# Optimization experiments

Measured on AMD Instinct MI355X. Metric: run time of the kernel, lower is better.

## Reference

```python
import jax, jax.numpy as jnp
import numpy as np


def setup_inputs() -> dict:
    key = jax.random.key(0)
    ks = jax.random.split(key, 8)
    B, S, V, E, H = 64, 128, 8000, 256, 512
    scale = 0.05
    return {
        "inputs": jax.random.randint(ks[0], (B, S), 0, V, dtype=jnp.int64),
        "embedding": jax.random.normal(ks[1], (V, E), dtype=jnp.float32) * scale,
        "W_ih": jax.random.normal(ks[2], (4 * H, E), dtype=jnp.float32) * scale,
        "W_hh": jax.random.normal(ks[3], (4 * H, H), dtype=jnp.float32) * scale,
        "b_ih": jax.random.normal(ks[4], (4 * H,), dtype=jnp.float32) * scale,
        "b_hh": jax.random.normal(ks[5], (4 * H,), dtype=jnp.float32) * scale,
        "W_cls": jax.random.normal(ks[6], (V, H), dtype=jnp.float32) * scale,
        "b_cls": jax.random.normal(ks[7], (V,), dtype=jnp.float32) * scale,
    }


def reference(inputs, embedding, W_ih, W_hh, b_ih, b_hh, W_cls, b_cls):
    B, S = inputs.shape
    H = W_hh.shape[1]
    x = embedding[inputs]  # (B, S, E)
    # batch the input-to-hidden GEMM across all timesteps
    x_gates = jnp.einsum('bse,ge->bsg', x, W_ih) + b_ih + b_hh  # (B, S, 4H)

    def step(carry, xg):
        h, c = carry
        gates = xg + h @ W_hh.T  # (B, 4H)
        i, f, g, o = jnp.split(gates, 4, axis=-1)  # PyTorch LSTMCell gate order
        i = jax.nn.sigmoid(i)
        f = jax.nn.sigmoid(f)
        g = jnp.tanh(g)
        o = jax.nn.sigmoid(o)
        c = f * c + i * g
        h = o * jnp.tanh(c)
        return (h, c), h

    h0 = jnp.zeros((B, H), dtype=x.dtype)
    c0 = jnp.zeros((B, H), dtype=x.dtype)
    _, hs = jax.lax.scan(step, (h0, c0), jnp.swapaxes(x_gates, 0, 1))  # hs: (S, B, H)
    hidden = jnp.swapaxes(hs, 0, 1)  # (B, S, H)
    logits = jnp.einsum('bsh,vh->bsv', hidden, W_cls) + b_cls  # (B, S, V)
    y = jnp.transpose(logits, (0, 2, 1))  # (B, V, S)
    return jax.nn.log_softmax(y, axis=1)
```

## Files before the change

kernel.cpp:

```cpp
#include <hip/hip_runtime.h>


using u16   = unsigned short;
using u32   = unsigned int;
using u16x8 = __attribute__((ext_vector_type(8))) u16;
using bf16x8 = __attribute__((ext_vector_type(8))) __bf16;
using f32x4 = __attribute__((ext_vector_type(4))) float;

#define NB   64
#define NS   128
#define NV   8000
#define NVP  8192
#define NE   256
#define NH   512
#define NG   2048
#define NBS  8192
#define OUT_BSTRIDE 1024000
#define XG_SSTRIDE  131072

__device__ inline u16 f2bf(float f) {
    unsigned x = __builtin_bit_cast(unsigned, f);
    unsigned r = (x + 0x7FFFu + ((x >> 16) & 1u)) >> 16;
    return (u16)r;
}

__device__ inline bf16x8 ld_frag(const u16* p) {
    u16x8 v = *(const u16x8*)p;
    return __builtin_bit_cast(bf16x8, v);
}

__device__ inline u32 load_llc(const u32* p) {
    u32 v;
    asm volatile("global_load_dword %0, %1, off sc0 sc1\n\t"
                 "s_waitcnt vmcnt(0)"
                 : "=v"(v) : "v"(p) : "memory");
    return v;
}
__device__ inline f32x4 load_llc16(const void* p) {
    f32x4 v;
    asm volatile("global_load_dwordx4 %0, %1, off sc0 sc1\n\t"
                 "s_waitcnt vmcnt(0)"
                 : "=v"(v) : "v"(p) : "memory");
    return v;
}
__device__ inline void store_llc(u32* p, u32 v) {
    asm volatile("global_store_dword %0, %1, off sc0 sc1"
                 :: "v"(p), "v"(v) : "memory");
}

__device__ inline void quad_transpose(float v[4], int p) {
    float tb[4];
    #pragma unroll
    for (int q2 = 0; q2 < 4; ++q2) tb[q2] = __shfl_xor(v[q2 ^ 2], 2);
    #pragma unroll
    for (int q2 = 0; q2 < 4; ++q2) v[q2] = (((q2 ^ p) & 2) ? tb[q2] : v[q2]);
    #pragma unroll
    for (int q2 = 0; q2 < 4; ++q2) tb[q2] = __shfl_xor(v[q2 ^ 1], 1);
    #pragma unroll
    for (int q2 = 0; q2 < 4; ++q2) v[q2] = (((q2 ^ p) & 1) ? tb[q2] : v[q2]);
}

__device__ inline float lstm_cell(const float v[4], float& c) {
    float i_ = 1.f / (1.f + __expf(-v[0]));
    float f_ = 1.f / (1.f + __expf(-v[1]));
    float e2 = __expf(2.f * v[2]);
    float g_ = 1.f - 2.f / (e2 + 1.f);
    float o_ = 1.f / (1.f + __expf(-v[3]));
    c = f_ * c + i_ * g_;
    float e2c = __expf(2.f * c);
    return o_ * (1.f - 2.f / (e2c + 1.f));
}

__global__ void cvt_bf16(const float* __restrict__ s, u16* __restrict__ d, int n8) {
    const float4* s4 = (const float4*)s;
    for (int i = blockIdx.x * blockDim.x + threadIdx.x; i < n8;
         i += gridDim.x * blockDim.x) {
        float4 a = s4[2 * i], b = s4[2 * i + 1];
        u16x8 o;
        o[0] = f2bf(a.x); o[1] = f2bf(a.y); o[2] = f2bf(a.z); o[3] = f2bf(a.w);
        o[4] = f2bf(b.x); o[5] = f2bf(b.y); o[6] = f2bf(b.z); o[7] = f2bf(b.w);
        ((u16x8*)d)[i] = o;
    }
}

__global__ __launch_bounds__(256) void k1_xgates(
    const u16* __restrict__ Wih, const u16* __restrict__ emb,
    const int* __restrict__ toks,
    const float* __restrict__ bih, const float* __restrict__ bhh,
    float* __restrict__ xg)
{
    __shared__ u16x8 Al8[512];
    __shared__ u16x8 Bl8[512];
    u16* Al = (u16*)Al8;
    u16* Bl = (u16*)Bl8;

    const int t = threadIdx.x;
    const int lane = t & 63, w = t >> 6;
    const int wm = w >> 1, wn = w & 1;
    const int gtile = blockIdx.y * 128, mtile = blockIdx.x * 128;

    const int r0 = t >> 2, r1 = r0 + 64, q = t & 3;
    const int m0 = mtile + r0, m1 = mtile + r1;
    const int tok0 = toks[(m0 & 63) * NS + (m0 >> 6)];
    const int tok1 = toks[(m1 & 63) * NS + (m1 >> 6)];

    f32x4 acc[4][4];
    for (int i = 0; i < 4; ++i)
        for (int j = 0; j < 4; ++j) acc[i][j] = {0.f, 0.f, 0.f, 0.f};

    const int kc8 = (lane >> 4) * 8;
    for (int kk = 0; kk < 8; ++kk) {
        const int k0 = kk * 32;
        *(u16x8*)&Al[t * 8]         = *(const u16x8*)&Wih[(gtile + r0) * NE + k0 + q * 8];
        *(u16x8*)&Al[(t + 256) * 8] = *(const u16x8*)&Wih[(gtile + r1) * NE + k0 + q * 8];
        *(u16x8*)&Bl[t * 8]         = *(const u16x8*)&emb[tok0 * NE + k0 + q * 8];
        *(u16x8*)&Bl[(t + 256) * 8] = *(const u16x8*)&emb[tok1 * NE + k0 + q * 8];
        __syncthreads();
        bf16x8 af[4], bf[4];
        #pragma unroll
        for (int i = 0; i < 4; ++i) {
            af[i] = ld_frag(&Al[(wm * 64 + i * 16 + (lane & 15)) * 32 + kc8]);
            bf[i] = ld_frag(&Bl[(wn * 64 + i * 16 + (lane & 15)) * 32 + kc8]);
        }
        #pragma unroll
        for (int fi = 0; fi < 4; ++fi)
            #pragma unroll
            for (int fj = 0; fj < 4; ++fj)
                acc[fi][fj] = __builtin_amdgcn_mfma_f32_16x16x32_bf16(
                    af[fi], bf[fj], acc[fi][fj], 0, 0, 0);
        __syncthreads();
    }

    #pragma unroll
    for (int fi = 0; fi < 4; ++fi) {
        const int g0 = gtile + wm * 64 + fi * 16 + ((lane >> 4) << 2);
        const float4 v1 = *(const float4*)&bih[g0];
        const float4 v2 = *(const float4*)&bhh[g0];
        float badd[4] = {v1.x + v2.x, v1.y + v2.y, v1.z + v2.z, v1.w + v2.w};
        #pragma unroll
        for (int fj = 0; fj < 4; ++fj) {
            const int m = mtile + wn * 64 + fj * 16 + (lane & 15);
            const int b = m & 63, s = m >> 6;
            float* dst = &xg[s * XG_SSTRIDE + b];
            #pragma unroll
            for (int r = 0; r < 4; ++r)
                dst[(g0 + r) * 64] = acc[fi][fj][r] + badd[r];
        }
    }
}

#define LSTM_NBLK 64

__global__ __launch_bounds__(512, 2) void k2_lstm(
    const u16* __restrict__ Whh,
    const float* __restrict__ xg,
    u16* __restrict__ hbuf,
    u16* __restrict__ hidden,
    u32* __restrict__ flags)
{
    __shared__ __align__(16) u16 hl[16 * 520];

    const int t = threadIdx.x, lane = t & 63, w = t >> 6;
    const int bg = blockIdx.x >> 3, ug = blockIdx.x & 7;
    const int j = lane & 15, kg = lane >> 4;
    const int kc8 = kg * 8;

    const int ubase = ug * 64 + w * 8;
    const int grow0 = (j & 3) * 512 + ubase + (j >> 2);
    const int grow1 = grow0 + 4;

    bf16x8 bw0[16], bw1[16];
    #pragma unroll
    for (int kk = 0; kk < 16; ++kk) {
        bw0[kk] = ld_frag(&Whh[grow0 * NH + kk * 32 + kc8]);
        bw1[kk] = ld_frag(&Whh[grow1 * NH + kk * 32 + kc8]);
    }
    #pragma unroll
    for (int kk = 0; kk < 16; ++kk) {
        f32x4 w0 = __builtin_bit_cast(f32x4, bw0[kk]);
        f32x4 w1 = __builtin_bit_cast(f32x4, bw1[kk]);
        asm volatile("" : "+v"(w0), "+v"(w1));
        bw0[kk] = __builtin_bit_cast(bf16x8, w0);
        bw1[kk] = __builtin_bit_cast(bf16x8, w1);
    }

    {
        u16x8 z = {0, 0, 0, 0, 0, 0, 0, 0};
        *(u16x8*)&hl[(8 + (t >> 6)) * 520 + (t & 63) * 8] = z;
    }

    const int srow = t >> 6;
    const int soff = (bg * 8 + srow) * NH + (t & 63) * 8;
    u16* hl_w = &hl[srow * 520 + (t & 63) * 8];

    const int p = lane & 3;
    const int q = (lane >> 2) & 3;
    const int batg = bg * 8 + (lane >> 4) * 4 + p;
    const int un0 = ubase + q;
    const bool act = lane < 32;
    const bool sl = act && ((lane & 4) == 0);

    const int xoff0 = grow0 * 64 + bg * 8 + (lane >> 4) * 4;
    const int xoff1 = grow1 * 64 + bg * 8 + (lane >> 4) * 4;

    float4 xv0 = {0, 0, 0, 0}, xv1 = {0, 0, 0, 0};
    if (act) {
        xv0 = *(const float4*)&xg[xoff0];
        xv1 = *(const float4*)&xg[xoff1];
    }
    float cA = 0.f, cB = 0.f;

    for (int step = 0; step < NS; ++step) {
        if (step > 0 && lane < 8) {
            const u32* fp = &flags[(bg * 8 + lane) * 32];
            while ((int)load_llc(fp) < step) __builtin_amdgcn_s_sleep(1);
        }
        {
            f32x4 hv = load_llc16(&hbuf[(step & 1) * (NB * NH) + soff]);
            *(f32x4*)hl_w = hv;
        }
        __syncthreads();

        float4 xn0 = {0, 0, 0, 0}, xn1 = {0, 0, 0, 0};
        if (act && step + 1 < NS) {
            const float* xb = &xg[(step + 1) * XG_SSTRIDE];
            xn0 = *(const float4*)&xb[xoff0];
            xn1 = *(const float4*)&xb[xoff1];
        }

        f32x4 a00 = {0, 0, 0, 0}, a01 = {0, 0, 0, 0};
        f32x4 a10 = {0, 0, 0, 0}, a11 = {0, 0, 0, 0};
        #pragma unroll
        for (int kk = 0; kk < 16; ++kk) {
            bf16x8 av = *(const bf16x8*)&hl[j * 520 + kk * 32 + kc8];
            if (kk & 1) {
                a01 = __builtin_amdgcn_mfma_f32_16x16x32_bf16(av, bw0[kk], a01, 0, 0, 0);
                a11 = __builtin_amdgcn_mfma_f32_16x16x32_bf16(av, bw1[kk], a11, 0, 0, 0);
            } else {
                a00 = __builtin_amdgcn_mfma_f32_16x16x32_bf16(av, bw0[kk], a00, 0, 0, 0);
                a10 = __builtin_amdgcn_mfma_f32_16x16x32_bf16(av, bw1[kk], a10, 0, 0, 0);
            }
        }

        float v0[4], v1[4];
        #pragma unroll
        for (int r = 0; r < 4; ++r) {
            v0[r] = a00[r] + a01[r] + (&xv0.x)[r];
            v1[r] = a10[r] + a11[r] + (&xv1.x)[r];
        }
        quad_transpose(v0, p);
        quad_transpose(v1, p);

        float h0 = lstm_cell(v0, cA);
        float h1 = lstm_cell(v1, cB);
        u32 hb0 = f2bf(h0), hb1 = f2bf(h1);
        u32 o0 = (u32)__shfl_xor((int)hb0, 4);
        u32 o1 = (u32)__shfl_xor((int)hb1, 4);
        if (sl) {
            u32 p0 = hb0 | (o0 << 16);
            u32 p1 = hb1 | (o1 << 16);
            u16* hn = hbuf + ((step & 1) ^ 1) * (NB * NH);
            store_llc((u32*)&hn[batg * NH + un0], p0);
            store_llc((u32*)&hn[batg * NH + un0 + 4], p1);
            *(u32*)&hidden[(batg * NS + step) * NH + un0] = p0;
            *(u32*)&hidden[(batg * NS + step) * NH + un0 + 4] = p1;
        }
        xv0 = xn0; xv1 = xn1;
        __syncthreads();

        if (step + 1 < NS && t == 0)
            store_llc(&flags[blockIdx.x * 32], (u32)(step + 1));
    }
}

__global__ __launch_bounds__(256) void k3_cls(
    const u16* __restrict__ Wc, const u16* __restrict__ hid,
    const float* __restrict__ bcls,
    float* __restrict__ out, float* __restrict__ lse)
{
    __shared__ u16x8 Al8[512];
    __shared__ u16x8 Bl8[512];
    __shared__ float red[2][128];
    u16* Al = (u16*)Al8;
    u16* Bl = (u16*)Bl8;

    const int t = threadIdx.x;
    const int lane = t & 63, w = t >> 6;
    const int wm = w >> 1, wn = w & 1;
    const int vtile = blockIdx.y * 128, mtile = blockIdx.x * 128;

    const int r0 = t >> 2, r1 = r0 + 64, q = t & 3;

    f32x4 acc[4][4];
    for (int i = 0; i < 4; ++i)
        for (int j2 = 0; j2 < 4; ++j2) acc[i][j2] = {0.f, 0.f, 0.f, 0.f};

    const int kc8 = (lane >> 4) * 8;
    for (int kk = 0; kk < 16; ++kk) {
        const int k0 = kk * 32;
        *(u16x8*)&Al[t * 8]         = *(const u16x8*)&Wc[(vtile + r0) * NH + k0 + q * 8];
        *(u16x8*)&Al[(t + 256) * 8] = *(const u16x8*)&Wc[(vtile + r1) * NH + k0 + q * 8];
        *(u16x8*)&Bl[t * 8]         = *(const u16x8*)&hid[(mtile + r0) * NH + k0 + q * 8];
        *(u16x8*)&Bl[(t + 256) * 8] = *(const u16x8*)&hid[(mtile + r1) * NH + k0 + q * 8];
        __syncthreads();
        bf16x8 af[4], bf[4];
        #pragma unroll
        for (int i = 0; i < 4; ++i) {
            af[i] = ld_frag(&Al[(wm * 64 + i * 16 + (lane & 15)) * 32 + kc8]);
            bf[i] = ld_frag(&Bl[(wn * 64 + i * 16 + (lane & 15)) * 32 + kc8]);
        }
        #pragma unroll
        for (int fi = 0; fi < 4; ++fi)
            #pragma unroll
            for (int fj = 0; fj < 4; ++fj)
                acc[fi][fj] = __builtin_amdgcn_mfma_f32_16x16x32_bf16(
                    af[fi], bf[fj], acc[fi][fj], 0, 0, 0);
        __syncthreads();
    }

    float lsum[4] = {0.f, 0.f, 0.f, 0.f};
    #pragma unroll
    for (int fi = 0; fi < 4; ++fi) {
        const int v0 = vtile + wm * 64 + fi * 16 + ((lane >> 4) << 2);
        const bool vok = (v0 < NV);
        float4 bc = {0.f, 0.f, 0.f, 0.f};
        if (vok) bc = *(const float4*)&bcls[v0];
        #pragma unroll
        for (int fj = 0; fj < 4; ++fj) {
            const int m = mtile + wn * 64 + fj * 16 + (lane & 15);
            const int b = m >> 7, s = m & 127;
            if (vok) {
                float* dst = &out[b * OUT_BSTRIDE + v0 * NS + s];
                float e = 0.f;
                #pragma unroll
                for (int r = 0; r < 4; ++r) {
                    float lg = acc[fi][fj][r] + (&bc.x)[r];
                    dst[r * NS] = lg;
                    e += __expf(lg);
                }
                lsum[fj] += e;
            }
        }
    }
    #pragma unroll
    for (int fj = 0; fj < 4; ++fj) {
        lsum[fj] += __shfl_xor(lsum[fj], 16);
        lsum[fj] += __shfl_xor(lsum[fj], 32);
    }
    if (lane < 16) {
        #pragma unroll
        for (int fj = 0; fj < 4; ++fj)
            red[wm][wn * 64 + fj * 16 + lane] = lsum[fj];
    }
    __syncthreads();
    if (t < 128) {
        const int m = mtile + t;
        atomicAdd(&lse[m], red[0][t] + red[1][t]);
    }
}

__global__ void k4_log(const float* __restrict__ lse, float* __restrict__ ll) {
    int i = blockIdx.x * 256 + threadIdx.x;
    if (i < NBS) ll[i] = logf(lse[i]);
}

__global__ void k5_norm(float* __restrict__ out, const float* __restrict__ ll) {
    const int total4 = NB * NV * NS / 4;
    float4* o4 = (float4*)out;
    for (int i = blockIdx.x * blockDim.x + threadIdx.x; i < total4;
         i += gridDim.x * blockDim.x) {
        const int i4 = i * 4;
        const int b = i4 / OUT_BSTRIDE;
        const int s = (i4 - b * OUT_BSTRIDE) & 127;
        float4 v = o4[i];
        const float4 l = *(const float4*)&ll[b * NS + s];
        v.x -= l.x; v.y -= l.y; v.z -= l.z; v.w -= l.w;
        o4[i] = v;
    }
}

extern "C" void kernel_launch(void* const* d_in, const int* in_sizes, int n_in,
                              void* d_out, int out_size, void* d_ws, size_t ws_size,
                              hipStream_t stream) {
    const int*   toks   = (const int*)d_in[0];
    const float* emb_f  = (const float*)d_in[1];
    const float* Wih_f  = (const float*)d_in[2];
    const float* Whh_f  = (const float*)d_in[3];
    const float* bih    = (const float*)d_in[4];
    const float* bhh    = (const float*)d_in[5];
    const float* Wcls_f = (const float*)d_in[6];
    const float* bcls   = (const float*)d_in[7];
    float* out = (float*)d_out;
    char*  ws  = (char*)d_ws;

    u32*   flags  = (u32*)(ws + 0);
    float* lse    = (float*)(ws + 8192);
    float* loglse = (float*)(ws + 40960);
    u16*   hbuf   = (u16*)(ws + 73728);
    u16*   embb   = (u16*)(ws + 204800);
    u16*   wihb   = (u16*)(ws + 4300800);
    u16*   whhb   = (u16*)(ws + 5349376);
    u16*   wclsb  = (u16*)(ws + 7446528);
    u16*   hidden = (u16*)(ws + 15835136);

    float* xg = out;

    hipMemsetAsync(ws, 0, 204800, stream);
    hipMemsetAsync((char*)wclsb + NV * NH * 2, 0, (NVP - NV) * NH * 2, stream);

    cvt_bf16<<<1024, 256, 0, stream>>>(emb_f,  embb,  NV * NE / 8);
    cvt_bf16<<<256,  256, 0, stream>>>(Wih_f,  wihb,  NG * NE / 8);
    cvt_bf16<<<512,  256, 0, stream>>>(Whh_f,  whhb,  NG * NH / 8);
    cvt_bf16<<<1024, 256, 0, stream>>>(Wcls_f, wclsb, NV * NH / 8);

    k1_xgates<<<dim3(64, 16), 256, 0, stream>>>(wihb, embb, toks, bih, bhh, xg);
    k2_lstm<<<LSTM_NBLK, 512, 0, stream>>>(whhb, xg, hbuf, hidden, flags);
    k3_cls<<<dim3(64, 64), 256, 0, stream>>>(wclsb, hidden, bcls, out, lse);
    k4_log<<<32, 256, 0, stream>>>(lse, loglse);
    k5_norm<<<2048, 256, 0, stream>>>(out, loglse);
}
```

Before: 668.5 us.

## Pack 16 batch rows per LSTM block to fill MFMA tiles, halving block count

The recurrent LSTM kernel now gives each block 16 batch rows instead of 8. Before, half of each 16-row MFMA A-tile was zero padding and half the lanes sat idle in the cell update. The grid shrinks from 64 to 32 cooperating blocks, and each thread now loads two hidden-state vectors per step through a combined LLC load. The LDS row stride also moves from 520 to 528 elements. The goal is less per-step sync and flag-polling overhead and better MFMA use, at the cost of more work per block on the serial critical path.

```diff
diff --git a/kernel.cpp b/kernel.cpp
--- a/kernel.cpp
+++ b/kernel.cpp
@@ -36,12 +36,12 @@
                  : "=v"(v) : "v"(p) : "memory");
     return v;
 }
-__device__ inline f32x4 load_llc16(const void* p) {
-    f32x4 v;
-    asm volatile("global_load_dwordx4 %0, %1, off sc0 sc1\n\t"
+__device__ inline void load_llc16x2(const void* p0, const void* p1,
+                                    f32x4& a, f32x4& b) {
+    asm volatile("global_load_dwordx4 %0, %2, off sc0 sc1\n\t"
+                 "global_load_dwordx4 %1, %3, off sc0 sc1\n\t"
                  "s_waitcnt vmcnt(0)"
-                 : "=v"(v) : "v"(p) : "memory");
-    return v;
+                 : "=&v"(a), "=&v"(b) : "v"(p0), "v"(p1) : "memory");
 }
 __device__ inline void store_llc(u32* p, u32 v) {
     asm volatile("global_store_dword %0, %1, off sc0 sc1"
@@ -149,21 +149,23 @@
     }
 }
 
-#define LSTM_NBLK 64
-
-__global__ __launch_bounds__(512, 2) void k2_lstm(
+#define LSTM_NBLK 32
+
+__global__ __attribute__((amdgpu_flat_work_group_size(512, 512),
+                          amdgpu_waves_per_eu(2, 2)))
+void k2_lstm(
     const u16* __restrict__ Whh,
     const float* __restrict__ xg,
     u16* __restrict__ hbuf,
     u16* __restrict__ hidden,
     u32* __restrict__ flags)
 {
-    __shared__ __align__(16) u16 hl[16 * 520];
+    __shared__ __align__(16) u16 hl[16 * 528];
 
     const int t = threadIdx.x, lane = t & 63, w = t >> 6;
     const int bg = blockIdx.x >> 3, ug = blockIdx.x & 7;
-    const int j = lane & 15, kg = lane >> 4;
-    const int kc8 = kg * 8;
+    const int j = lane & 15;
+    const int kc8 = (lane >> 4) * 8;
 
     const int ubase = ug * 64 + w * 8;
     const int grow0 = (j & 3) * 512 + ubase + (j >> 2);
@@ -184,30 +186,23 @@
         bw1[kk] = __builtin_bit_cast(bf16x8, w1);
     }
 
-    {
-        u16x8 z = {0, 0, 0, 0, 0, 0, 0, 0};
-        *(u16x8*)&hl[(8 + (t >> 6)) * 520 + (t & 63) * 8] = z;
-    }
-
-    const int srow = t >> 6;
-    const int soff = (bg * 8 + srow) * NH + (t & 63) * 8;
-    u16* hl_w = &hl[srow * 520 + (t & 63) * 8];
-
-    const int p = lane & 3;
-    const int q = (lane >> 2) & 3;
-    const int batg = bg * 8 + (lane >> 4) * 4 + p;
+    const int srow = t >> 5;
+    const int sc   = (t & 31) * 8;
+    const int soff = (bg * 16 + srow) * NH + sc;
+    u16* hl_w = &hl[srow * 528 + sc];
+
+    const int p  = lane & 3;
+    const int q  = (lane >> 2) & 3;
+    const int mb = (lane >> 4) * 4;
+    const int bat = bg * 16 + mb + p;
     const int un0 = ubase + q;
-    const bool act = lane < 32;
-    const bool sl = act && ((lane & 4) == 0);
-
-    const int xoff0 = grow0 * 64 + bg * 8 + (lane >> 4) * 4;
-    const int xoff1 = grow1 * 64 + bg * 8 + (lane >> 4) * 4;
-
-    float4 xv0 = {0, 0, 0, 0}, xv1 = {0, 0, 0, 0};
-    if (act) {
-        xv0 = *(const float4*)&xg[xoff0];
-        xv1 = *(const float4*)&xg[xoff1];
-    }
+    const bool sl = ((lane & 4) == 0);
+
+    const int xoff0 = grow0 * 64 + bg * 16 + mb;
+    const int xoff1 = grow1 * 64 + bg * 16 + mb;
+
+    float4 xv0 = *(const float4*)&xg[xoff0];
+    float4 xv1 = *(const float4*)&xg[xoff1];
     float cA = 0.f, cB = 0.f;
 
     for (int step = 0; step < NS; ++step) {
@@ -216,13 +211,16 @@
             while ((int)load_llc(fp) < step) __builtin_amdgcn_s_sleep(1);
         }
         {
-            f32x4 hv = load_llc16(&hbuf[(step & 1) * (NB * NH) + soff]);
-            *(f32x4*)hl_w = hv;
+            const u16* hsrc = hbuf + (step & 1) * (NB * NH) + soff;
+            f32x4 hA, hB;
+            load_llc16x2(hsrc, hsrc + 256, hA, hB);
+            *(f32x4*)hl_w = hA;
+            *(f32x4*)(hl_w + 256) = hB;
         }
         __syncthreads();
 
         float4 xn0 = {0, 0, 0, 0}, xn1 = {0, 0, 0, 0};
-        if (act && step + 1 < NS) {
+        if (step + 1 < NS) {
             const float* xb = &xg[(step + 1) * XG_SSTRIDE];
             xn0 = *(const float4*)&xb[xoff0];
             xn1 = *(const float4*)&xb[xoff1];
@@ -232,7 +230,7 @@
         f32x4 a10 = {0, 0, 0, 0}, a11 = {0, 0, 0, 0};
         #pragma unroll
         for (int kk = 0; kk < 16; ++kk) {
-            bf16x8 av = *(const bf16x8*)&hl[j * 520 + kk * 32 + kc8];
+            bf16x8 av = *(const bf16x8*)&hl[j * 528 + kk * 32 + kc8];
             if (kk & 1) {
                 a01 = __builtin_amdgcn_mfma_f32_16x16x32_bf16(av, bw0[kk], a01, 0, 0, 0);
                 a11 = __builtin_amdgcn_mfma_f32_16x16x32_bf16(av, bw1[kk], a11, 0, 0, 0);
@@ -260,10 +258,10 @@
             u32 p0 = hb0 | (o0 << 16);
             u32 p1 = hb1 | (o1 << 16);
             u16* hn = hbuf + ((step & 1) ^ 1) * (NB * NH);
-            store_llc((u32*)&hn[batg * NH + un0], p0);
-            store_llc((u32*)&hn[batg * NH + un0 + 4], p1);
-            *(u32*)&hidden[(batg * NS + step) * NH + un0] = p0;
-            *(u32*)&hidden[(batg * NS + step) * NH + un0 + 4] = p1;
+            store_llc((u32*)&hn[bat * NH + un0], p0);
+            store_llc((u32*)&hn[bat * NH + un0 + 4], p1);
+            *(u32*)&hidden[(bat * NS + step) * NH + un0] = p0;
+            *(u32*)&hidden[(bat * NS + step) * NH + un0 + 4] = p1;
         }
         xv0 = xn0; xv1 = xn1;
         __syncthreads();
```

After: 711.5 us. 1.06x slower.

## Restructure LSTM recurrence loop with two-step xg prefetch and single barrier

Applied to the files above, without the earlier changes.

Unrolls the recurrent LSTM loop by two and prefetches the input-gate values two steps ahead with raw async loads into alternating registers. The two __syncthreads per step become one hand-written waitcnt plus s_barrier. The completion flag is now published before the hidden-sequence stores, and step 0 skips the recurrent MFMA because h is zero. LDS row padding changes from 520 to 528, and the workspace memset shrinks because hbuf no longer needs zeroing. The aim is to shorten the serial per-step critical path, at the cost of correctness depending on the manual vmcnt accounting.

```diff
diff --git a/kernel.cpp b/kernel.cpp
--- a/kernel.cpp
+++ b/kernel.cpp
@@ -47,6 +47,10 @@
     asm volatile("global_store_dword %0, %1, off sc0 sc1"
                  :: "v"(p), "v"(v) : "memory");
 }
+__device__ inline void prefetch16(f32x4& d, const float* p) {
+    asm volatile("global_load_dwordx4 %0, %1, off"
+                 : "=v"(d) : "v"(p) : "memory");
+}
 
 __device__ inline void quad_transpose(float v[4], int p) {
     float tb[4];
@@ -158,7 +162,7 @@
     u16* __restrict__ hidden,
     u32* __restrict__ flags)
 {
-    __shared__ __align__(16) u16 hl[16 * 520];
+    __shared__ __align__(16) u16 hl[16 * 528];
 
     const int t = threadIdx.x, lane = t & 63, w = t >> 6;
     const int bg = blockIdx.x >> 3, ug = blockIdx.x & 7;
@@ -186,67 +190,65 @@
 
     {
         u16x8 z = {0, 0, 0, 0, 0, 0, 0, 0};
-        *(u16x8*)&hl[(8 + (t >> 6)) * 520 + (t & 63) * 8] = z;
-    }
-
-    const int srow = t >> 6;
-    const int soff = (bg * 8 + srow) * NH + (t & 63) * 8;
-    u16* hl_w = &hl[srow * 520 + (t & 63) * 8];
-
-    const int p = lane & 3;
-    const int q = (lane >> 2) & 3;
-    const int batg = bg * 8 + (lane >> 4) * 4 + p;
+        *(u16x8*)&hl[(8 + (t >> 6)) * 528 + (t & 63) * 8] = z;
+    }
+
+    const int srow = t >> 6, scol = (t & 63) * 8;
+    const int soff = (bg * 8 + srow) * NH + scol;
+    u16* hl_w = &hl[srow * 528 + scol];
+
+    const int p  = lane & 3;
+    const int q  = (lane >> 2) & 3;
+    const int mb = kg * 4;
+    const bool real = (kg < 2);
+    const int bat = bg * 8 + mb + p;
     const int un0 = ubase + q;
-    const bool act = lane < 32;
-    const bool sl = act && ((lane & 4) == 0);
-
-    const int xoff0 = grow0 * 64 + bg * 8 + (lane >> 4) * 4;
-    const int xoff1 = grow1 * 64 + bg * 8 + (lane >> 4) * 4;
-
-    float4 xv0 = {0, 0, 0, 0}, xv1 = {0, 0, 0, 0};
-    if (act) {
-        xv0 = *(const float4*)&xg[xoff0];
-        xv1 = *(const float4*)&xg[xoff1];
+    const bool sl = real && ((lane & 4) == 0);
+
+    const int xo0 = grow0 * 64 + bg * 8 + mb;
+    const int xo1 = grow1 * 64 + bg * 8 + mb;
+
+    f32x4 xvA0 = {0,0,0,0}, xvA1 = {0,0,0,0};
+    f32x4 xvB0 = {0,0,0,0}, xvB1 = {0,0,0,0};
+    if (real) {
+        xvA0 = *(const f32x4*)&xg[xo0];
+        xvA1 = *(const f32x4*)&xg[xo1];
+        xvB0 = *(const f32x4*)&xg[XG_SSTRIDE + xo0];
+        xvB1 = *(const f32x4*)&xg[XG_SSTRIDE + xo1];
     }
     float cA = 0.f, cB = 0.f;
 
-    for (int step = 0; step < NS; ++step) {
-        if (step > 0 && lane < 8) {
-            const u32* fp = &flags[(bg * 8 + lane) * 32];
-            while ((int)load_llc(fp) < step) __builtin_amdgcn_s_sleep(1);
-        }
-        {
+    auto body = [&](int step, f32x4& X0, f32x4& X1) {
+        f32x4 a00 = {0,0,0,0}, a01 = {0,0,0,0};
+        f32x4 a10 = {0,0,0,0}, a11 = {0,0,0,0};
+
+        if (step > 0) {
+            if (lane < 8) {
+                const u32* fp = &flags[(bg * 8 + lane) * 32];
+                while ((int)load_llc(fp) < step) __builtin_amdgcn_s_sleep(1);
+            }
             f32x4 hv = load_llc16(&hbuf[(step & 1) * (NB * NH) + soff]);
             *(f32x4*)hl_w = hv;
-        }
-        __syncthreads();
-
-        float4 xn0 = {0, 0, 0, 0}, xn1 = {0, 0, 0, 0};
-        if (act && step + 1 < NS) {
-            const float* xb = &xg[(step + 1) * XG_SSTRIDE];
-            xn0 = *(const float4*)&xb[xoff0];
-            xn1 = *(const float4*)&xb[xoff1];
-        }
-
-        f32x4 a00 = {0, 0, 0, 0}, a01 = {0, 0, 0, 0};
-        f32x4 a10 = {0, 0, 0, 0}, a11 = {0, 0, 0, 0};
-        #pragma unroll
-        for (int kk = 0; kk < 16; ++kk) {
-            bf16x8 av = *(const bf16x8*)&hl[j * 520 + kk * 32 + kc8];
-            if (kk & 1) {
-                a01 = __builtin_amdgcn_mfma_f32_16x16x32_bf16(av, bw0[kk], a01, 0, 0, 0);
-                a11 = __builtin_amdgcn_mfma_f32_16x16x32_bf16(av, bw1[kk], a11, 0, 0, 0);
-            } else {
-                a00 = __builtin_amdgcn_mfma_f32_16x16x32_bf16(av, bw0[kk], a00, 0, 0, 0);
-                a10 = __builtin_amdgcn_mfma_f32_16x16x32_bf16(av, bw1[kk], a10, 0, 0, 0);
+            __syncthreads();
+
+            #pragma unroll
+            for (int kk = 0; kk < 16; ++kk) {
+                bf16x8 av = *(const bf16x8*)&hl[j * 528 + kk * 32 + kc8];
+                if (kk & 1) {
+                    a01 = __builtin_amdgcn_mfma_f32_16x16x32_bf16(av, bw0[kk], a01, 0, 0, 0);
+                    a11 = __builtin_amdgcn_mfma_f32_16x16x32_bf16(av, bw1[kk], a11, 0, 0, 0);
+                } else {
+                    a00 = __builtin_amdgcn_mfma_f32_16x16x32_bf16(av, bw0[kk], a00, 0, 0, 0);
+                    a10 = __builtin_amdgcn_mfma_f32_16x16x32_bf16(av, bw1[kk], a10, 0, 0, 0);
+                }
             }
         }
 
         float v0[4], v1[4];
         #pragma unroll
         for (int r = 0; r < 4; ++r) {
-            v0[r] = a00[r] + a01[r] + (&xv0.x)[r];
-            v1[r] = a10[r] + a11[r] + (&xv1.x)[r];
+            v0[r] = a00[r] + a01[r] + X0[r];
+            v1[r] = a10[r] + a11[r] + X1[r];
         }
         quad_transpose(v0, p);
         quad_transpose(v1, p);
@@ -256,20 +258,34 @@
         u32 hb0 = f2bf(h0), hb1 = f2bf(h1);
         u32 o0 = (u32)__shfl_xor((int)hb0, 4);
         u32 o1 = (u32)__shfl_xor((int)hb1, 4);
-        if (sl) {
-            u32 p0 = hb0 | (o0 << 16);
-            u32 p1 = hb1 | (o1 << 16);
-            u16* hn = hbuf + ((step & 1) ^ 1) * (NB * NH);
-            store_llc((u32*)&hn[batg * NH + un0], p0);
-            store_llc((u32*)&hn[batg * NH + un0 + 4], p1);
-            *(u32*)&hidden[(batg * NS + step) * NH + un0] = p0;
-            *(u32*)&hidden[(batg * NS + step) * NH + un0 + 4] = p1;
-        }
-        xv0 = xn0; xv1 = xn1;
-        __syncthreads();
-
+        u32 pr0 = hb0 | (o0 << 16);
+        u32 pr1 = hb1 | (o1 << 16);
+
+        if (step + 1 < NS && sl) {
+            u32* hp = (u32*)&hbuf[((step + 1) & 1) * (NB * NH) + bat * NH + un0];
+            store_llc(hp, pr0);
+            store_llc(hp + 2, pr1);
+        }
+        if (step + 2 < NS && real) {
+            const float* xb = &xg[(step + 2) * XG_SSTRIDE];
+            prefetch16(X0, &xb[xo0]);
+            prefetch16(X1, &xb[xo1]);
+        }
+        if (step + 2 < NS)
+            asm volatile("s_waitcnt vmcnt(2) lgkmcnt(0)\n\ts_barrier" ::: "memory");
+        else
+            asm volatile("s_waitcnt vmcnt(0) lgkmcnt(0)\n\ts_barrier" ::: "memory");
         if (step + 1 < NS && t == 0)
             store_llc(&flags[blockIdx.x * 32], (u32)(step + 1));
+        if (sl) {
+            *(u32*)&hidden[(bat * NS + step) * NH + un0] = pr0;
+            *(u32*)&hidden[(bat * NS + step) * NH + un0 + 4] = pr1;
+        }
+    };
+
+    for (int s2 = 0; s2 < NS / 2; ++s2) {
+        body(2 * s2,     xvA0, xvA1);
+        body(2 * s2 + 1, xvB0, xvB1);
     }
 }
 
@@ -405,7 +421,7 @@
 
     float* xg = out;
 
-    hipMemsetAsync(ws, 0, 204800, stream);
+    hipMemsetAsync(ws, 0, 73728, stream);
     hipMemsetAsync((char*)wclsb + NV * NH * 2, 0, (NVP - NV) * NH * 2, stream);
 
     cvt_bf16<<<1024, 256, 0, stream>>>(emb_f,  embb,  NV * NE / 8);
```

After: 684.3 us. 1.02x slower.

## Prefetch xg earlier, defer hidden stores, pad LDS, use direct global-to-LDS loads

Applied to the files above, without the earlier changes.

In the LSTM recurrence kernel, the next step's input-gate loads are issued as asm loads at the top of the step, before the flag spin-wait, so their latency overlaps the wait. The non-critical stores to the hidden-state output are moved after the flag release so they no longer delay the signal to other blocks. The LDS row stride for h is padded from 520 to 528 elements. In the classifier GEMM, register-staged global loads into LDS are replaced with global_load_lds direct-to-LDS transfers. This may race, since the asm prefetch result is read without an explicit wait and the direct-LDS loads depend on the existing __syncthreads for ordering.

```diff
diff --git a/kernel.cpp b/kernel.cpp
--- a/kernel.cpp
+++ b/kernel.cpp
@@ -47,6 +47,17 @@
     asm volatile("global_store_dword %0, %1, off sc0 sc1"
                  :: "v"(p), "v"(v) : "memory");
 }
+__device__ inline void prefetch16(f32x4& d, const float* p) {
+    asm volatile("global_load_dwordx4 %0, %1, off"
+                 : "=v"(d) : "v"(p) : "memory");
+}
+
+__device__ inline void gload_lds16(const u16* g, u16* l) {
+    __builtin_amdgcn_global_load_lds(
+        (const __attribute__((address_space(1))) unsigned int*)(const void*)g,
+        (__attribute__((address_space(3))) unsigned int*)(void*)l,
+        16, 0, 0);
+}
 
 __device__ inline void quad_transpose(float v[4], int p) {
     float tb[4];
@@ -158,12 +169,12 @@
     u16* __restrict__ hidden,
     u32* __restrict__ flags)
 {
-    __shared__ __align__(16) u16 hl[16 * 520];
+    __shared__ __align__(16) u16 hl[16 * 528];
 
     const int t = threadIdx.x, lane = t & 63, w = t >> 6;
     const int bg = blockIdx.x >> 3, ug = blockIdx.x & 7;
-    const int j = lane & 15, kg = lane >> 4;
-    const int kc8 = kg * 8;
+    const int j = lane & 15;
+    const int kc8 = (lane >> 4) * 8;
 
     const int ubase = ug * 64 + w * 8;
     const int grow0 = (j & 3) * 512 + ubase + (j >> 2);
@@ -186,12 +197,12 @@
 
     {
         u16x8 z = {0, 0, 0, 0, 0, 0, 0, 0};
-        *(u16x8*)&hl[(8 + (t >> 6)) * 520 + (t & 63) * 8] = z;
-    }
-
-    const int srow = t >> 6;
-    const int soff = (bg * 8 + srow) * NH + (t & 63) * 8;
-    u16* hl_w = &hl[srow * 520 + (t & 63) * 8];
+        *(u16x8*)&hl[(8 + (t >> 6)) * 528 + (t & 63) * 8] = z;
+    }
+
+    const int srow = t >> 6, scol = (t & 63) * 8;
+    const int soff = (bg * 8 + srow) * NH + scol;
+    u16* hl_w = &hl[srow * 528 + scol];
 
     const int p = lane & 3;
     const int q = (lane >> 2) & 3;
@@ -203,14 +214,20 @@
     const int xoff0 = grow0 * 64 + bg * 8 + (lane >> 4) * 4;
     const int xoff1 = grow1 * 64 + bg * 8 + (lane >> 4) * 4;
 
-    float4 xv0 = {0, 0, 0, 0}, xv1 = {0, 0, 0, 0};
+    f32x4 xv0 = {0, 0, 0, 0}, xv1 = {0, 0, 0, 0};
+    f32x4 xn0 = {0, 0, 0, 0}, xn1 = {0, 0, 0, 0};
     if (act) {
-        xv0 = *(const float4*)&xg[xoff0];
-        xv1 = *(const float4*)&xg[xoff1];
+        xv0 = *(const f32x4*)&xg[xoff0];
+        xv1 = *(const f32x4*)&xg[xoff1];
     }
     float cA = 0.f, cB = 0.f;
 
     for (int step = 0; step < NS; ++step) {
+        if (act && step + 1 < NS) {
+            const float* xb = &xg[(step + 1) * XG_SSTRIDE];
+            prefetch16(xn0, &xb[xoff0]);
+            prefetch16(xn1, &xb[xoff1]);
+        }
         if (step > 0 && lane < 8) {
             const u32* fp = &flags[(bg * 8 + lane) * 32];
             while ((int)load_llc(fp) < step) __builtin_amdgcn_s_sleep(1);
@@ -221,18 +238,11 @@
         }
         __syncthreads();
 
-        float4 xn0 = {0, 0, 0, 0}, xn1 = {0, 0, 0, 0};
-        if (act && step + 1 < NS) {
-            const float* xb = &xg[(step + 1) * XG_SSTRIDE];
-            xn0 = *(const float4*)&xb[xoff0];
-            xn1 = *(const float4*)&xb[xoff1];
-        }
-
         f32x4 a00 = {0, 0, 0, 0}, a01 = {0, 0, 0, 0};
         f32x4 a10 = {0, 0, 0, 0}, a11 = {0, 0, 0, 0};
         #pragma unroll
         for (int kk = 0; kk < 16; ++kk) {
-            bf16x8 av = *(const bf16x8*)&hl[j * 520 + kk * 32 + kc8];
+            bf16x8 av = *(const bf16x8*)&hl[j * 528 + kk * 32 + kc8];
             if (kk & 1) {
                 a01 = __builtin_amdgcn_mfma_f32_16x16x32_bf16(av, bw0[kk], a01, 0, 0, 0);
                 a11 = __builtin_amdgcn_mfma_f32_16x16x32_bf16(av, bw1[kk], a11, 0, 0, 0);
@@ -245,8 +255,8 @@
         float v0[4], v1[4];
         #pragma unroll
         for (int r = 0; r < 4; ++r) {
-            v0[r] = a00[r] + a01[r] + (&xv0.x)[r];
-            v1[r] = a10[r] + a11[r] + (&xv1.x)[r];
+            v0[r] = a00[r] + a01[r] + xv0[r];
+            v1[r] = a10[r] + a11[r] + xv1[r];
         }
         quad_transpose(v0, p);
         quad_transpose(v1, p);
@@ -256,20 +266,24 @@
         u32 hb0 = f2bf(h0), hb1 = f2bf(h1);
         u32 o0 = (u32)__shfl_xor((int)hb0, 4);
         u32 o1 = (u32)__shfl_xor((int)hb1, 4);
+        u32 pr0 = hb0 | (o0 << 16);
+        u32 pr1 = hb1 | (o1 << 16);
+
         if (sl) {
-            u32 p0 = hb0 | (o0 << 16);
-            u32 p1 = hb1 | (o1 << 16);
             u16* hn = hbuf + ((step & 1) ^ 1) * (NB * NH);
-            store_llc((u32*)&hn[batg * NH + un0], p0);
-            store_llc((u32*)&hn[batg * NH + un0 + 4], p1);
-            *(u32*)&hidden[(batg * NS + step) * NH + un0] = p0;
-            *(u32*)&hidden[(batg * NS + step) * NH + un0 + 4] = p1;
+            store_llc((u32*)&hn[batg * NH + un0], pr0);
+            store_llc((u32*)&hn[batg * NH + un0 + 4], pr1);
         }
         xv0 = xn0; xv1 = xn1;
         __syncthreads();
 
         if (step + 1 < NS && t == 0)
             store_llc(&flags[blockIdx.x * 32], (u32)(step + 1));
+
+        if (sl) {
+            *(u32*)&hidden[(batg * NS + step) * NH + un0] = pr0;
+            *(u32*)&hidden[(batg * NS + step) * NH + un0 + 4] = pr1;
+        }
     }
 }
 
@@ -278,18 +292,23 @@
     const float* __restrict__ bcls,
     float* __restrict__ out, float* __restrict__ lse)
 {
-    __shared__ u16x8 Al8[512];
-    __shared__ u16x8 Bl8[512];
+    __shared__ __align__(16) u16 Al[128 * 32];
+    __shared__ __align__(16) u16 Bl[128 * 32];
     __shared__ float red[2][128];
-    u16* Al = (u16*)Al8;
-    u16* Bl = (u16*)Bl8;
 
     const int t = threadIdx.x;
     const int lane = t & 63, w = t >> 6;
     const int wm = w >> 1, wn = w & 1;
     const int vtile = blockIdx.y * 128, mtile = blockIdx.x * 128;
 
-    const int r0 = t >> 2, r1 = r0 + 64, q = t & 3;
+    const int srow = w * 16 + (lane >> 2);
+    const int scol = (lane & 3) * 8;
+    const u16* gA = &Wc[(vtile + srow) * NH + scol];
+    const u16* gB = &hid[(mtile + srow) * NH + scol];
+    u16* lA0 = &Al[(w * 16) * 32];
+    u16* lA1 = &Al[(w * 16 + 64) * 32];
+    u16* lB0 = &Bl[(w * 16) * 32];
+    u16* lB1 = &Bl[(w * 16 + 64) * 32];
 
     f32x4 acc[4][4];
     for (int i = 0; i < 4; ++i)
@@ -298,10 +317,10 @@
     const int kc8 = (lane >> 4) * 8;
     for (int kk = 0; kk < 16; ++kk) {
         const int k0 = kk * 32;
-        *(u16x8*)&Al[t * 8]         = *(const u16x8*)&Wc[(vtile + r0) * NH + k0 + q * 8];
-        *(u16x8*)&Al[(t + 256) * 8] = *(const u16x8*)&Wc[(vtile + r1) * NH + k0 + q * 8];
-        *(u16x8*)&Bl[t * 8]         = *(const u16x8*)&hid[(mtile + r0) * NH + k0 + q * 8];
-        *(u16x8*)&Bl[(t + 256) * 8] = *(const u16x8*)&hid[(mtile + r1) * NH + k0 + q * 8];
+        gload_lds16(gA + k0,           lA0);
+        gload_lds16(gA + 64 * NH + k0, lA1);
+        gload_lds16(gB + k0,           lB0);
+        gload_lds16(gB + 64 * NH + k0, lB1);
         __syncthreads();
         bf16x8 af[4], bf[4];
         #pragma unroll
```

Result: faster. 626.4 us (-6.3%).
